# Kernel optimization log

Measured on AMD Instinct MI355X. Metric: run time of the kernel, lower is better.

Reference implementation:

```python
import jax, jax.numpy as jnp
import numpy as np

IMG_H, IMG_W = 240, 320
NEAR, FAR = 0.1, 10.0
CHUNK = 64  # triangles rasterized per scan step
CAM_K = np.array([[286.2057, 0.0, 162.6306],
                  [0.0, 286.7852, 121.0245],
                  [0.0, 0.0, 1.0]], np.float32)


def build_projection(cam, w, h, x0=0, y0=0, nc=NEAR, fc=FAR):
    q = -(fc + nc) / float(fc - nc)
    qn = -2.0 * fc * nc / float(fc - nc)
    proj = np.array([
        [2 * cam[0, 0] / w, -2 * cam[0, 1] / w, (-2 * cam[0, 2] + w + 2 * x0) / w, 0],
        [0, -2 * cam[1, 1] / h, (-2 * cam[1, 2] + h + 2 * y0) / h, 0],
        [0, 0, q, qn],
        [0, 0, -1, 0]], dtype=np.float64)
    proj[1, :] *= -1.0
    return jnp.asarray(proj.T, jnp.float32)


def vertex_normals(verts, faces):
    # per-face normal scattered to its vertices then renormalized
    # (equals dirt lighting.vertex_normals_pre_split on split meshes)
    v0, v1, v2 = verts[faces[:, 0]], verts[faces[:, 1]], verts[faces[:, 2]]
    fn = jnp.cross(v1 - v0, v2 - v0)
    fn = fn / jnp.maximum(jnp.linalg.norm(fn, axis=1, keepdims=True), 1e-12)
    vn = (jnp.zeros_like(verts)
          .at[faces[:, 0]].add(fn)
          .at[faces[:, 1]].add(fn)
          .at[faces[:, 2]].add(fn))
    return vn / jnp.maximum(jnp.linalg.norm(vn, axis=1, keepdims=True), 1e-12)


def transform_vertices(vertices, pose, faces, proj):
    vert_obj = jnp.concatenate([vertices, jnp.ones_like(vertices[:, -1:])], axis=1)  # [V,4]
    normals = vertex_normals(vert_obj[:, :3], faces)
    gl = jnp.array([[1., 0., 0.], [0., -1., 0.], [0., 0., -1.]], jnp.float32)
    rot = gl @ pose[:3, :3]
    # replicate the flat-list surgery: cam_pose[:3,:3]=gl@R, negate t_y, t_z
    cam_pose = pose.at[:3, :3].set(rot).at[1, 3].multiply(-1.0).at[2, 3].multiply(-1.0)
    view = cam_pose.T
    vert_cam = vert_obj @ view                                   # [V,4]
    vert_3d = vert_obj[:, :3] @ pose[:3, :3].T + pose[:3, 3]     # [V,3]
    vert_clip = vert_cam @ proj                                  # [V,4]
    return vert_obj, vert_3d, vert_clip, normals


def rasterise(vert_clip, colors, faces, H, W):
    # z-buffered triangle rasterization with perspective-correct barycentric
    # interpolation, processed in chunks of CHUNK triangles via lax.scan.
    eps = 1e-9
    wc = vert_clip[:, 3]
    inv_w = 1.0 / jnp.where(jnp.abs(wc) > eps, wc, eps)
    ndc = vert_clip[:, :3] * inv_w[:, None]
    px = (ndc[:, 0] + 1.0) * 0.5 * W   # screen x
    py = (1.0 - ndc[:, 1]) * 0.5 * H   # screen y (row 0 at top)
    pz = ndc[:, 2]

    tpx, tpy, tpz = px[faces], py[faces], pz[faces]   # [F,3]
    tiw = inv_w[faces]                                # [F,3]
    tcol = colors[faces]                              # [F,3,C]
    tval = jnp.all(wc[faces] > 1e-6, axis=1)          # all verts in front

    F = faces.shape[0]
    pad = (-F) % CHUNK
    def padf(a):
        if pad == 0:
            return a
        return jnp.concatenate([a, jnp.zeros((pad,) + a.shape[1:], a.dtype)], 0)
    tpx, tpy, tpz, tiw, tcol = padf(tpx), padf(tpy), padf(tpz), padf(tiw), padf(tcol)
    tval = padf(tval)
    n_steps = (F + pad) // CHUNK
    resh = lambda a: a.reshape((n_steps, CHUNK) + a.shape[1:])
    xs = tuple(map(resh, (tpx, tpy, tpz, tiw, tcol, tval)))

    Xg = (jnp.arange(W, dtype=jnp.float32) + 0.5)[None, :, None]  # pixel centers
    Yg = (jnp.arange(H, dtype=jnp.float32) + 0.5)[:, None, None]
    BIG = jnp.float32(1e9)

    def step(carry, chunk):
        zbuf, cbuf = carry
        cpx, cpy, cpz, ciw, ccol, cval = chunk
        ax, ay = cpx[:, 0], cpy[:, 0]
        bx, by = cpx[:, 1], cpy[:, 1]
        cx, cy = cpx[:, 2], cpy[:, 2]
        area = (bx - ax) * (cy - ay) - (by - ay) * (cx - ax)            # [Fc]
        inv_area = 1.0 / jnp.where(jnp.abs(area) > 1e-12, area, 1e-12)
        # normalized edge functions (barycentrics), [H,W,Fc]
        e0 = ((Xg - bx) * (cy - by) - (Yg - by) * (cx - bx)) * inv_area
        e1 = ((Xg - cx) * (ay - cy) - (Yg - cy) * (ax - cx)) * inv_area
        e2 = 1.0 - e0 - e1
        depth = e0 * cpz[:, 0] + e1 * cpz[:, 1] + e2 * cpz[:, 2]        # screen-linear z
        inside = ((e0 >= 0) & (e1 >= 0) & (e2 >= 0) & cval
                  & (jnp.abs(area) > 1e-12) & (depth >= -1.0) & (depth <= 1.0))
        dmask = jnp.where(inside, depth, BIG)
        best = jnp.argmin(dmask, axis=2)                                # [H,W]
        bidx = best[..., None]
        bdepth = jnp.take_along_axis(dmask, bidx, 2)[..., 0]
        take = bdepth < zbuf
        b0 = jnp.take_along_axis(e0, bidx, 2)[..., 0]
        b1 = jnp.take_along_axis(e1, bidx, 2)[..., 0]
        b2 = 1.0 - b0 - b1
        piw = jnp.stack([b0, b1, b2], -1) * ciw[best]                   # [H,W,3]
        den = jnp.sum(piw, -1, keepdims=True)
        den = jnp.where(jnp.abs(den) > 1e-12, den, 1e-12)
        col = jnp.einsum('hwk,hwkc->hwc', piw / den, ccol[best])        # persp-correct
        zbuf = jnp.where(take, bdepth, zbuf)
        cbuf = jnp.where(take[..., None], col, cbuf)
        return (zbuf, cbuf), None

    zbuf0 = jnp.full((H, W), BIG, jnp.float32)
    cbuf0 = jnp.zeros((H, W, colors.shape[1]), jnp.float32)
    (_, cbuf), _ = jax.lax.scan(jax.checkpoint(step), (zbuf0, cbuf0), xs)
    return cbuf


def setup_inputs() -> dict:
    key = jax.random.key(0)
    k1, k2 = jax.random.split(key)
    V, F = 12288, 4096
    vertices = 0.15 * jax.random.normal(k1, (1, V, 3), jnp.float32)
    faces = jax.random.randint(k2, (1, F, 3), 0, V, jnp.int32)
    pose = jnp.eye(4, dtype=jnp.float32).at[2, 3].set(0.6)  # object 0.6m in front
    return {"vertices": vertices, "faces": faces, "poses": pose[None]}


def reference(vertices, faces, poses):
    proj = build_projection(CAM_K, IMG_W, IMG_H)
    faces0 = jnp.asarray(faces[0], jnp.int32)
    vert_obj, vert_3d, vert_clip, normals = transform_vertices(vertices[0], poses[0], faces0, proj)
    colors = jnp.concatenate(
        [jnp.ones_like(vert_obj[:, :1]), vert_3d, normals, vert_obj], axis=1)  # [V,11]
    g = rasterise(vert_clip, colors, faces0, IMG_H, IMG_W)  # [H,W,11]
    return g[None]
```

## Files before the change

kernel.cpp:

```cpp
#include <hip/hip_runtime.h>
#include <math.h>

#pragma clang fp contract(off)

#define IMG_H 240
#define IMG_W 320
#define NPX   (IMG_H * IMG_W)
#define NCH   11
#define NCHP  12
#define NSLICE 16
#define CULL_M 1e-3f
#define EZ_M   1e-5f

struct ProjM { float m[16]; };

extern "C" __global__ void k_init(float* __restrict__ vnacc, int n3v,
                                  unsigned long long* __restrict__ zkey) {
  int i = blockIdx.x * 256 + threadIdx.x;
  if (i < n3v) vnacc[i] = 0.0f;
  if (i < NPX) zkey[i] = ~0ull;
}

__device__ __forceinline__ void xform(float x, float y, float z,
                                      const float* __restrict__ pose,
                                      const ProjM& P,
                                      float& px, float& py, float& pz,
                                      float& iw, float& wc) {
  float c0 = ((x*pose[0]     + y*pose[1])     + z*pose[2])     + pose[3];
  float c1 = ((x*(-pose[4])  + y*(-pose[5]))  + z*(-pose[6]))  + (-pose[7]);
  float c2 = ((x*(-pose[8])  + y*(-pose[9]))  + z*(-pose[10])) + (-pose[11]);
  float c3 = ((x*pose[12]    + y*pose[13])    + z*pose[14])    + pose[15];
  float q0 = ((c0*P.m[0]  + c1*P.m[1])  + c2*P.m[2])  + c3*P.m[3];
  float q1 = ((c0*P.m[4]  + c1*P.m[5])  + c2*P.m[6])  + c3*P.m[7];
  float q2 = ((c0*P.m[8]  + c1*P.m[9])  + c2*P.m[10]) + c3*P.m[11];
  float q3 = ((c0*P.m[12] + c1*P.m[13]) + c2*P.m[14]) + c3*P.m[15];
  wc = q3;
  float denw = (fabsf(wc) > 1e-9f) ? wc : 1e-9f;
  iw = 1.0f / denw;
  float ndx = q0 * iw, ndy = q1 * iw;
  pz = q2 * iw;
  px = ((ndx + 1.0f) * 0.5f) * (float)IMG_W;
  py = ((1.0f - ndy) * 0.5f) * (float)IMG_H;
}

extern "C" __global__ void k_face(const float* __restrict__ verts,
                                  const int* __restrict__ faces,
                                  const float* __restrict__ pose,
                                  ProjM P,
                                  float* __restrict__ vnacc,
                                  float4* __restrict__ frec,
                                  float4* __restrict__ fbb,
                                  float4* __restrict__ fe,
                                  int4*  __restrict__ fidx, int F) {
  int f = blockIdx.x * 64 + threadIdx.x;
  if (f >= F) return;
  int i0 = faces[3*f+0], i1 = faces[3*f+1], i2 = faces[3*f+2];
  float x0 = verts[3*i0+0], y0 = verts[3*i0+1], z0 = verts[3*i0+2];
  float x1 = verts[3*i1+0], y1 = verts[3*i1+1], z1 = verts[3*i1+2];
  float x2 = verts[3*i2+0], y2 = verts[3*i2+1], z2 = verts[3*i2+2];

  {
    float ux = x1 - x0, uy = y1 - y0, uz = z1 - z0;
    float vx = x2 - x0, vy = y2 - y0, vz = z2 - z0;
    float fx = uy*vz - uz*vy;
    float fy = uz*vx - ux*vz;
    float fz = ux*vy - uy*vx;
    float n = sqrtf((fx*fx + fy*fy) + fz*fz);
    float d = fmaxf(n, 1e-12f);
    fx = fx / d; fy = fy / d; fz = fz / d;
    atomicAdd(&vnacc[3*i0+0], fx); atomicAdd(&vnacc[3*i0+1], fy); atomicAdd(&vnacc[3*i0+2], fz);
    atomicAdd(&vnacc[3*i1+0], fx); atomicAdd(&vnacc[3*i1+1], fy); atomicAdd(&vnacc[3*i1+2], fz);
    atomicAdd(&vnacc[3*i2+0], fx); atomicAdd(&vnacc[3*i2+1], fy); atomicAdd(&vnacc[3*i2+2], fz);
  }

  float ax, ay, pz0, iw0, w0;  xform(x0, y0, z0, pose, P, ax, ay, pz0, iw0, w0);
  float bx, by, pz1, iw1, w1;  xform(x1, y1, z1, pose, P, bx, by, pz1, iw1, w1);
  float cx, cy, pz2, iw2, w2;  xform(x2, y2, z2, pose, P, cx, cy, pz2, iw2, w2);

  float area = (bx - ax) * (cy - ay) - (by - ay) * (cx - ax);
  float inva = 1.0f / ((fabsf(area) > 1e-12f) ? area : 1e-12f);
  bool valid = (w0 > 1e-6f) && (w1 > 1e-6f) && (w2 > 1e-6f) && (fabsf(area) > 1e-12f);
  float rax = 2.0f*cx - ax, ray = 2.0f*cy - ay;
  float rbx = 2.0f*cx - bx, rby = 2.0f*cy - by;
  float minx = fminf(cx, fminf(rax, rbx)), maxx = fmaxf(cx, fmaxf(rax, rbx));
  float miny = fminf(cy, fminf(ray, rby)), maxy = fmaxf(cy, fmaxf(ray, rby));
  frec[4*f+0] = make_float4(bx, by, cy - by, cx - bx);
  frec[4*f+1] = make_float4(cx, cy, ay - cy, ax - cx);
  frec[4*f+2] = make_float4(inva, pz0, pz1, pz2);
  frec[4*f+3] = make_float4(iw0, iw1, iw2, 0.0f);
  fbb[f] = valid ? make_float4(minx, maxx, miny, maxy)
                 : make_float4(1e30f, -1e30f, 1e30f, -1e30f);
  fidx[f] = make_int4(i0, i1, i2, 0);
  {
    double dbx = bx, dby = by, dcx = cx, dcy = cy, dax = ax, day = ay;
    double dinv = (double)inva;
    double d0 = dcy - dby, d1 = dcx - dbx;
    double d2 = day - dcy, d3 = dax - dcx;
    double a0 = d0 * dinv, b0 = -d1 * dinv, c0 = (dby * d1 - dbx * d0) * dinv;
    double a1 = d2 * dinv, b1 = -d3 * dinv, c1 = (dcy * d3 - dcx * d2) * dinv;
    fe[2*f+0] = make_float4((float)a0, (float)b0, (float)c0, 0.0f);
    fe[2*f+1] = make_float4((float)a1, (float)b1, (float)c1, 0.0f);
  }
}

extern "C" __global__ void k_vertex(const float* __restrict__ verts,
                                    const float* __restrict__ vnacc,
                                    const float* __restrict__ pose,
                                    float4* __restrict__ colors, int V) {
  int i = blockIdx.x * 64 + threadIdx.x;
  if (i >= V) return;
  float x = verts[3*i+0], y = verts[3*i+1], z = verts[3*i+2];

  float nx = vnacc[3*i+0], ny = vnacc[3*i+1], nz = vnacc[3*i+2];
  float nn = sqrtf((nx*nx + ny*ny) + nz*nz);
  float nm = fmaxf(nn, 1e-12f);
  nx = nx / nm; ny = ny / nm; nz = nz / nm;

  float v3x = ((x*pose[0] + y*pose[1]) + z*pose[2])  + pose[3];
  float v3y = ((x*pose[4] + y*pose[5]) + z*pose[6])  + pose[7];
  float v3z = ((x*pose[8] + y*pose[9]) + z*pose[10]) + pose[11];

  colors[3*i+0] = make_float4(1.0f, v3x, v3y, v3z);
  colors[3*i+1] = make_float4(nx, ny, nz, x);
  colors[3*i+2] = make_float4(y, z, 1.0f, 0.0f);
}

extern "C" __global__ __launch_bounds__(256)
void k_rasterA(const float4* __restrict__ frec,
               const float4* __restrict__ fbb,
               const float4* __restrict__ fe,
               unsigned long long* __restrict__ zkey,
               int F, int nslice) {
  int t = threadIdx.x;
  int wave = t >> 6;
  int lane = t & 63;
  int sx = (wave & 1) * 8, sy = (wave >> 1) * 8;
  int pxi = blockIdx.x * 16 + sx + (lane & 7);
  int pyi = blockIdx.y * 16 + sy + (lane >> 3);
  float X = (float)pxi + 0.5f;
  float Y = (float)pyi + 0.5f;
  float tXlo = (float)(blockIdx.x * 16 + sx) + 0.5f, tXhi = tXlo + 7.0f;
  float tYlo = (float)(blockIdx.y * 16 + sy) + 0.5f, tYhi = tYlo + 7.0f;

  int f0 = blockIdx.z * nslice;
  int f1 = min(F, f0 + nslice);

  float bestd = 1e9f;
  int   besti = -1;

  for (int base = f0; base < f1; base += 64) {
    int f = base + lane;
    bool ov = false;
    if (f < f1) {
      float4 bb = fbb[f];
      ov = (bb.x - 1.0f <= tXhi) && (bb.y + 1.0f >= tXlo) &&
           (bb.z - 1.0f <= tYhi) && (bb.w + 1.0f >= tYlo);
      if (ov) {
        float4 E0 = fe[2*f+0];
        float4 E1 = fe[2*f+1];
        float pa0 = E0.x * tXlo, pb0 = E0.x * tXhi;
        float qa0 = E0.y * tYlo, qb0 = E0.y * tYhi;
        float e0mx = (fmaxf(pa0, pb0) + fmaxf(qa0, qb0)) + E0.z;
        float e0mn = (fminf(pa0, pb0) + fminf(qa0, qb0)) + E0.z;
        float pa1 = E1.x * tXlo, pb1 = E1.x * tXhi;
        float qa1 = E1.y * tYlo, qb1 = E1.y * tYhi;
        float e1mx = (fmaxf(pa1, pb1) + fmaxf(qa1, qb1)) + E1.z;
        float e1mn = (fminf(pa1, pb1) + fminf(qa1, qb1)) + E1.z;
        float e2mx = (1.0f - e0mn) - e1mn;
        ov = (e0mx >= -CULL_M) && (e1mx >= -CULL_M) && (e2mx >= -CULL_M);
      }
    }
    unsigned long long mask = __ballot(ov);

    while (mask) {
      int j0 = __builtin_ctzll(mask);
      mask &= mask - 1;
      bool two = (mask != 0ull);
      int j1 = two ? __builtin_ctzll(mask) : j0;
      if (two) mask &= mask - 1;

      int ju0 = __builtin_amdgcn_readfirstlane(base + j0);
      int ju1 = __builtin_amdgcn_readfirstlane(base + j1);
      const float4* fr0 = frec + (size_t)ju0 * 4;
      const float4* fr1 = frec + (size_t)ju1 * 4;
      float4 C0 = fr0[2];
      float4 C1 = fr1[2];
      float zmin0 = fminf(C0.y, fminf(C0.z, C0.w));
      float zmin1 = fminf(C1.y, fminf(C1.z, C1.w));
      float zmg = two ? fminf(zmin0, zmin1) : zmin0;
      if (__ballot(bestd > zmg - EZ_M) == 0ull) continue;
      float4 A0 = fr0[0], B0 = fr0[1];
      float4 A1 = fr1[0], B1 = fr1[1];

      {
        float t0 = (X - A0.x) * A0.z;
        float t1 = (Y - A0.y) * A0.w;
        float e0 = (t0 - t1) * C0.x;
        float t2 = (X - B0.x) * B0.z;
        float t3 = (Y - B0.y) * B0.w;
        float e1 = (t2 - t3) * C0.x;
        float e2 = (1.0f - e0) - e1;
        float depth = ((e0 * C0.y) + (e1 * C0.z)) + (e2 * C0.w);
        bool inside = (e0 >= 0.0f) && (e1 >= 0.0f) && (e2 >= 0.0f) &&
                      (depth >= -1.0f) && (depth <= 1.0f);
        if (inside && depth < bestd) { bestd = depth; besti = ju0; }
      }
      if (two) {
        float t0 = (X - A1.x) * A1.z;
        float t1 = (Y - A1.y) * A1.w;
        float e0 = (t0 - t1) * C1.x;
        float t2 = (X - B1.x) * B1.z;
        float t3 = (Y - B1.y) * B1.w;
        float e1 = (t2 - t3) * C1.x;
        float e2 = (1.0f - e0) - e1;
        float depth = ((e0 * C1.y) + (e1 * C1.z)) + (e2 * C1.w);
        bool inside = (e0 >= 0.0f) && (e1 >= 0.0f) && (e2 >= 0.0f) &&
                      (depth >= -1.0f) && (depth <= 1.0f);
        if (inside && depth < bestd) { bestd = depth; besti = ju1; }
      }
    }
  }

  if (besti >= 0) {
    unsigned int ub = __float_as_uint(bestd);
    ub = (ub & 0x80000000u) ? ~ub : (ub | 0x80000000u);
    unsigned long long key = ((unsigned long long)ub << 32) | (unsigned int)besti;
    atomicMin(&zkey[(size_t)pyi * IMG_W + pxi], key);
  }
}

extern "C" __global__ __launch_bounds__(256)
void k_resolve(const unsigned long long* __restrict__ zkey,
               const float4* __restrict__ frec,
               const float4* __restrict__ colors,
               const int4* __restrict__ fidx,
               float* __restrict__ out) {
  __shared__ float sOut[256 * NCH];
  int t = threadIdx.x;
  int p = blockIdx.x * 256 + t;
  int pyi = p / IMG_W, pxi = p - pyi * IMG_W;
  float X = (float)pxi + 0.5f;
  float Y = (float)pyi + 0.5f;
  unsigned long long key = zkey[p];

  float oc[NCH];
  if (key != ~0ull) {
    int besti = (int)(key & 0xFFFFFFFFu);
    const float4* fr = frec + (size_t)besti * 4;
    float4 A = fr[0], B = fr[1], C = fr[2], D = fr[3];
    float t0 = (X - A.x) * A.z;
    float t1 = (Y - A.y) * A.w;
    float e0 = (t0 - t1) * C.x;
    float t2 = (X - B.x) * B.z;
    float t3 = (Y - B.y) * B.w;
    float e1 = (t2 - t3) * C.x;
    float b2 = (1.0f - e0) - e1;
    float p0 = e0 * D.x, p1 = e1 * D.y, p2 = b2 * D.z;
    float den = (p0 + p1) + p2;
    if (!(fabsf(den) > 1e-12f)) den = 1e-12f;
    float u0 = p0 / den, u1 = p1 / den, u2 = p2 / den;
    int4 vi = fidx[besti];
    float c0v[NCHP], c1v[NCHP], c2v[NCHP];
    #pragma unroll
    for (int k = 0; k < 3; ++k) {
      *(float4*)(c0v + 4*k) = colors[3*vi.x + k];
      *(float4*)(c1v + 4*k) = colors[3*vi.y + k];
      *(float4*)(c2v + 4*k) = colors[3*vi.z + k];
    }
    #pragma unroll
    for (int ch = 0; ch < NCH; ++ch)
      oc[ch] = (u0 * c0v[ch] + u1 * c1v[ch]) + u2 * c2v[ch];
  } else {
    #pragma unroll
    for (int ch = 0; ch < NCH; ++ch) oc[ch] = 0.0f;
  }
  #pragma unroll
  for (int ch = 0; ch < NCH; ++ch) sOut[t * NCH + ch] = oc[ch];
  __syncthreads();
  float4* o4 = (float4*)(out + (size_t)blockIdx.x * 256 * NCH);
  const float4* s4 = (const float4*)sOut;
  #pragma unroll
  for (int k = 0; k < 3; ++k) {
    int idx = t + k * 256;
    if (idx < 704) o4[idx] = s4[idx];
  }
}

extern "C" void kernel_launch(void* const* d_in, const int* in_sizes, int n_in,
                              void* d_out, int out_size, void* d_ws, size_t ws_size,
                              hipStream_t stream) {
  const float* verts = (const float*)d_in[0];
  const int*   faces = (const int*)d_in[1];
  const float* pose  = (const float*)d_in[2];
  float* out = (float*)d_out;
  int V = in_sizes[0] / 3;
  int F = in_sizes[1] / 3;

  float* ws = (float*)d_ws;
  size_t o = 0;
  auto alloc = [&](size_t n) { size_t r = o; o += (n + 3) & ~(size_t)3; return r; };
  size_t o_zk   = alloc((size_t)2 * NPX);
  size_t o_vn   = alloc((size_t)3 * V);
  size_t o_col  = alloc((size_t)NCHP * V);
  size_t o_fr   = alloc((size_t)16 * F);
  size_t o_bb   = alloc((size_t)4 * F);
  size_t o_fe   = alloc((size_t)8 * F);
  size_t o_fi   = alloc((size_t)4 * F);
  unsigned long long* zkey = (unsigned long long*)(ws + o_zk);
  float*  vnacc = ws + o_vn;
  float4* col   = (float4*)(ws + o_col);
  float4* frec  = (float4*)(ws + o_fr);
  float4* fbb   = (float4*)(ws + o_bb);
  float4* fe    = (float4*)(ws + o_fe);
  int4*   fidx  = (int4*)(ws + o_fi);

  double fxd = 286.2057, sd = 0.0, cxd = 162.6306;
  double fyd = 286.7852, cyd = 121.0245;
  double wd = IMG_W, hd = IMG_H, ncd = 0.1, fcd = 10.0;
  double q  = -(fcd + ncd) / (fcd - ncd);
  double qn = -2.0 * fcd * ncd / (fcd - ncd);
  double Pd[16] = {
    2.0*fxd/wd, -2.0*sd/wd, (-2.0*cxd + wd)/wd, 0.0,
    0.0,        2.0*fyd/hd, (2.0*cyd - hd)/hd, -0.0,
    0.0,        0.0,        q,                  qn,
    0.0,        0.0,       -1.0,                0.0 };
  ProjM P;
  for (int i = 0; i < 16; ++i) P.m[i] = (float)Pd[i];

  int n3v = 3 * V;
  int initN = (NPX > n3v) ? NPX : n3v;
  k_init<<<(initN + 255) / 256, 256, 0, stream>>>(vnacc, n3v, zkey);
  k_face<<<(F + 63) / 64, 64, 0, stream>>>(verts, faces, pose, P, vnacc,
                                           frec, fbb, fe, fidx, F);
  k_vertex<<<(V + 63) / 64, 64, 0, stream>>>(verts, vnacc, pose, col, V);
  int nslice = (F + NSLICE - 1) / NSLICE;
  dim3 g(IMG_W / 16, IMG_H / 16, NSLICE);
  k_rasterA<<<g, 256, 0, stream>>>(frec, fbb, fe, zkey, F, nslice);
  k_resolve<<<NPX / 256, 256, 0, stream>>>(zkey, frec, col, fidx, out);
}
```

Baseline: 90.64 us.

## Add block-level face binning in rasterizer and fuse vertex attributes into resolve

The rasterizer now culls faces once per 16x16 block using all 256 threads, compacts the survivors into a shared-memory list, and then has each 8x8 wave re-test only that short list. The face slice count drops from 16 to 4, so each block handles more faces and fewer blocks are launched. The separate vertex-color kernel is removed and the resolve kernel computes normalized normals and pose-transformed positions on the fly for the three vertices it needs. This saves one launch and the color buffer traffic, at the cost of extra __syncthreads per batch, repeated per-pixel vertex math, and less grid parallelism.

```diff
diff --git a/kernel.cpp b/kernel.cpp
--- a/kernel.cpp
+++ b/kernel.cpp
@@ -7,8 +7,7 @@
 #define IMG_W 320
 #define NPX   (IMG_H * IMG_W)
 #define NCH   11
-#define NCHP  12
-#define NSLICE 16
+#define NSLICE 4
 #define CULL_M 1e-3f
 #define EZ_M   1e-5f
 
@@ -103,34 +102,14 @@
   }
 }
 
-extern "C" __global__ void k_vertex(const float* __restrict__ verts,
-                                    const float* __restrict__ vnacc,
-                                    const float* __restrict__ pose,
-                                    float4* __restrict__ colors, int V) {
-  int i = blockIdx.x * 64 + threadIdx.x;
-  if (i >= V) return;
-  float x = verts[3*i+0], y = verts[3*i+1], z = verts[3*i+2];
-
-  float nx = vnacc[3*i+0], ny = vnacc[3*i+1], nz = vnacc[3*i+2];
-  float nn = sqrtf((nx*nx + ny*ny) + nz*nz);
-  float nm = fmaxf(nn, 1e-12f);
-  nx = nx / nm; ny = ny / nm; nz = nz / nm;
-
-  float v3x = ((x*pose[0] + y*pose[1]) + z*pose[2])  + pose[3];
-  float v3y = ((x*pose[4] + y*pose[5]) + z*pose[6])  + pose[7];
-  float v3z = ((x*pose[8] + y*pose[9]) + z*pose[10]) + pose[11];
-
-  colors[3*i+0] = make_float4(1.0f, v3x, v3y, v3z);
-  colors[3*i+1] = make_float4(nx, ny, nz, x);
-  colors[3*i+2] = make_float4(y, z, 1.0f, 0.0f);
-}
-
 extern "C" __global__ __launch_bounds__(256)
 void k_rasterA(const float4* __restrict__ frec,
                const float4* __restrict__ fbb,
                const float4* __restrict__ fe,
                unsigned long long* __restrict__ zkey,
                int F, int nslice) {
+  __shared__ int sList[256];
+  __shared__ int sWaveCnt[4];
   int t = threadIdx.x;
   int wave = t >> 6;
   int lane = t & 63;
@@ -141,6 +120,8 @@
   float Y = (float)pyi + 0.5f;
   float tXlo = (float)(blockIdx.x * 16 + sx) + 0.5f, tXhi = tXlo + 7.0f;
   float tYlo = (float)(blockIdx.y * 16 + sy) + 0.5f, tYhi = tYlo + 7.0f;
+  float bXlo = (float)(blockIdx.x * 16) + 0.5f, bXhi = bXlo + 15.0f;
+  float bYlo = (float)(blockIdx.y * 16) + 0.5f, bYhi = bYlo + 15.0f;
 
   int f0 = blockIdx.z * nslice;
   int f1 = min(F, f0 + nslice);
@@ -148,77 +129,115 @@
   float bestd = 1e9f;
   int   besti = -1;
 
-  for (int base = f0; base < f1; base += 64) {
-    int f = base + lane;
-    bool ov = false;
+  for (int base = f0; base < f1; base += 256) {
+    int f = base + t;
+    bool bp = false;
     if (f < f1) {
       float4 bb = fbb[f];
-      ov = (bb.x - 1.0f <= tXhi) && (bb.y + 1.0f >= tXlo) &&
-           (bb.z - 1.0f <= tYhi) && (bb.w + 1.0f >= tYlo);
-      if (ov) {
+      bp = (bb.x - 1.0f <= bXhi) && (bb.y + 1.0f >= bXlo) &&
+           (bb.z - 1.0f <= bYhi) && (bb.w + 1.0f >= bYlo);
+      if (bp) {
         float4 E0 = fe[2*f+0];
         float4 E1 = fe[2*f+1];
-        float pa0 = E0.x * tXlo, pb0 = E0.x * tXhi;
-        float qa0 = E0.y * tYlo, qb0 = E0.y * tYhi;
+        float pa0 = E0.x * bXlo, pb0 = E0.x * bXhi;
+        float qa0 = E0.y * bYlo, qb0 = E0.y * bYhi;
         float e0mx = (fmaxf(pa0, pb0) + fmaxf(qa0, qb0)) + E0.z;
         float e0mn = (fminf(pa0, pb0) + fminf(qa0, qb0)) + E0.z;
-        float pa1 = E1.x * tXlo, pb1 = E1.x * tXhi;
-        float qa1 = E1.y * tYlo, qb1 = E1.y * tYhi;
+        float pa1 = E1.x * bXlo, pb1 = E1.x * bXhi;
+        float qa1 = E1.y * bYlo, qb1 = E1.y * bYhi;
         float e1mx = (fmaxf(pa1, pb1) + fmaxf(qa1, qb1)) + E1.z;
         float e1mn = (fminf(pa1, pb1) + fminf(qa1, qb1)) + E1.z;
         float e2mx = (1.0f - e0mn) - e1mn;
-        ov = (e0mx >= -CULL_M) && (e1mx >= -CULL_M) && (e2mx >= -CULL_M);
+        bp = (e0mx >= -CULL_M) && (e1mx >= -CULL_M) && (e2mx >= -CULL_M);
       }
     }
-    unsigned long long mask = __ballot(ov);
-
-    while (mask) {
-      int j0 = __builtin_ctzll(mask);
-      mask &= mask - 1;
-      bool two = (mask != 0ull);
-      int j1 = two ? __builtin_ctzll(mask) : j0;
-      if (two) mask &= mask - 1;
-
-      int ju0 = __builtin_amdgcn_readfirstlane(base + j0);
-      int ju1 = __builtin_amdgcn_readfirstlane(base + j1);
-      const float4* fr0 = frec + (size_t)ju0 * 4;
-      const float4* fr1 = frec + (size_t)ju1 * 4;
-      float4 C0 = fr0[2];
-      float4 C1 = fr1[2];
-      float zmin0 = fminf(C0.y, fminf(C0.z, C0.w));
-      float zmin1 = fminf(C1.y, fminf(C1.z, C1.w));
-      float zmg = two ? fminf(zmin0, zmin1) : zmin0;
-      if (__ballot(bestd > zmg - EZ_M) == 0ull) continue;
-      float4 A0 = fr0[0], B0 = fr0[1];
-      float4 A1 = fr1[0], B1 = fr1[1];
-
-      {
-        float t0 = (X - A0.x) * A0.z;
-        float t1 = (Y - A0.y) * A0.w;
-        float e0 = (t0 - t1) * C0.x;
-        float t2 = (X - B0.x) * B0.z;
-        float t3 = (Y - B0.y) * B0.w;
-        float e1 = (t2 - t3) * C0.x;
-        float e2 = (1.0f - e0) - e1;
-        float depth = ((e0 * C0.y) + (e1 * C0.z)) + (e2 * C0.w);
-        bool inside = (e0 >= 0.0f) && (e1 >= 0.0f) && (e2 >= 0.0f) &&
-                      (depth >= -1.0f) && (depth <= 1.0f);
-        if (inside && depth < bestd) { bestd = depth; besti = ju0; }
+    unsigned long long wm = __ballot(bp);
+    if (lane == 0) sWaveCnt[wave] = __popcll(wm);
+    __syncthreads();
+    int c0 = sWaveCnt[0], c1 = sWaveCnt[1], c2 = sWaveCnt[2], c3 = sWaveCnt[3];
+    int tot = ((c0 + c1) + c2) + c3;
+    if (bp) {
+      int off = (wave > 0 ? c0 : 0) + (wave > 1 ? c1 : 0) + (wave > 2 ? c2 : 0);
+      int pos = off + __popcll(wm & ((1ull << lane) - 1ull));
+      sList[pos] = f;
+    }
+    __syncthreads();
+
+    for (int k0 = 0; k0 < tot; k0 += 64) {
+      int k = k0 + lane;
+      bool ov = false;
+      int fi = 0;
+      if (k < tot) {
+        fi = sList[k];
+        float4 bb = fbb[fi];
+        ov = (bb.x - 1.0f <= tXhi) && (bb.y + 1.0f >= tXlo) &&
+             (bb.z - 1.0f <= tYhi) && (bb.w + 1.0f >= tYlo);
+        if (ov) {
+          float4 E0 = fe[2*fi+0];
+          float4 E1 = fe[2*fi+1];
+          float pa0 = E0.x * tXlo, pb0 = E0.x * tXhi;
+          float qa0 = E0.y * tYlo, qb0 = E0.y * tYhi;
+          float e0mx = (fmaxf(pa0, pb0) + fmaxf(qa0, qb0)) + E0.z;
+          float e0mn = (fminf(pa0, pb0) + fminf(qa0, qb0)) + E0.z;
+          float pa1 = E1.x * tXlo, pb1 = E1.x * tXhi;
+          float qa1 = E1.y * tYlo, qb1 = E1.y * tYhi;
+          float e1mx = (fmaxf(pa1, pb1) + fmaxf(qa1, qb1)) + E1.z;
+          float e1mn = (fminf(pa1, pb1) + fminf(qa1, qb1)) + E1.z;
+          float e2mx = (1.0f - e0mn) - e1mn;
+          ov = (e0mx >= -CULL_M) && (e1mx >= -CULL_M) && (e2mx >= -CULL_M);
+        }
       }
-      if (two) {
-        float t0 = (X - A1.x) * A1.z;
-        float t1 = (Y - A1.y) * A1.w;
-        float e0 = (t0 - t1) * C1.x;
-        float t2 = (X - B1.x) * B1.z;
-        float t3 = (Y - B1.y) * B1.w;
-        float e1 = (t2 - t3) * C1.x;
-        float e2 = (1.0f - e0) - e1;
-        float depth = ((e0 * C1.y) + (e1 * C1.z)) + (e2 * C1.w);
-        bool inside = (e0 >= 0.0f) && (e1 >= 0.0f) && (e2 >= 0.0f) &&
-                      (depth >= -1.0f) && (depth <= 1.0f);
-        if (inside && depth < bestd) { bestd = depth; besti = ju1; }
+      unsigned long long mask = __ballot(ov);
+
+      while (mask) {
+        int j0 = __builtin_ctzll(mask);
+        mask &= mask - 1;
+        bool two = (mask != 0ull);
+        int j1 = two ? __builtin_ctzll(mask) : j0;
+        if (two) mask &= mask - 1;
+
+        int ju0 = __builtin_amdgcn_readfirstlane(__shfl(fi, j0));
+        int ju1 = __builtin_amdgcn_readfirstlane(__shfl(fi, j1));
+        const float4* fr0 = frec + (size_t)ju0 * 4;
+        const float4* fr1 = frec + (size_t)ju1 * 4;
+        float4 C0 = fr0[2];
+        float4 C1 = fr1[2];
+        float zmin0 = fminf(C0.y, fminf(C0.z, C0.w));
+        float zmin1 = fminf(C1.y, fminf(C1.z, C1.w));
+        float zmg = two ? fminf(zmin0, zmin1) : zmin0;
+        if (__ballot(bestd > zmg - EZ_M) == 0ull) continue;
+        float4 A0 = fr0[0], B0 = fr0[1];
+        float4 A1 = fr1[0], B1 = fr1[1];
+
+        {
+          float t0 = (X - A0.x) * A0.z;
+          float t1 = (Y - A0.y) * A0.w;
+          float e0 = (t0 - t1) * C0.x;
+          float t2 = (X - B0.x) * B0.z;
+          float t3 = (Y - B0.y) * B0.w;
+          float e1 = (t2 - t3) * C0.x;
+          float e2 = (1.0f - e0) - e1;
+          float depth = ((e0 * C0.y) + (e1 * C0.z)) + (e2 * C0.w);
+          bool inside = (e0 >= 0.0f) && (e1 >= 0.0f) && (e2 >= 0.0f) &&
+                        (depth >= -1.0f) && (depth <= 1.0f);
+          if (inside && depth < bestd) { bestd = depth; besti = ju0; }
+        }
+        if (two) {
+          float t0 = (X - A1.x) * A1.z;
+          float t1 = (Y - A1.y) * A1.w;
+          float e0 = (t0 - t1) * C1.x;
+          float t2 = (X - B1.x) * B1.z;
+          float t3 = (Y - B1.y) * B1.w;
+          float e1 = (t2 - t3) * C1.x;
+          float e2 = (1.0f - e0) - e1;
+          float depth = ((e0 * C1.y) + (e1 * C1.z)) + (e2 * C1.w);
+          bool inside = (e0 >= 0.0f) && (e1 >= 0.0f) && (e2 >= 0.0f) &&
+                        (depth >= -1.0f) && (depth <= 1.0f);
+          if (inside && depth < bestd) { bestd = depth; besti = ju1; }
+        }
       }
     }
+    __syncthreads();
   }
 
   if (besti >= 0) {
@@ -232,8 +251,10 @@
 extern "C" __global__ __launch_bounds__(256)
 void k_resolve(const unsigned long long* __restrict__ zkey,
                const float4* __restrict__ frec,
-               const float4* __restrict__ colors,
                const int4* __restrict__ fidx,
+               const float* __restrict__ verts,
+               const float* __restrict__ vnacc,
+               const float* __restrict__ pose,
                float* __restrict__ out) {
   __shared__ float sOut[256 * NCH];
   int t = threadIdx.x;
@@ -260,16 +281,27 @@
     if (!(fabsf(den) > 1e-12f)) den = 1e-12f;
     float u0 = p0 / den, u1 = p1 / den, u2 = p2 / den;
     int4 vi = fidx[besti];
-    float c0v[NCHP], c1v[NCHP], c2v[NCHP];
+
+    float cv[3][NCH];
+    int vids[3] = { vi.x, vi.y, vi.z };
     #pragma unroll
     for (int k = 0; k < 3; ++k) {
-      *(float4*)(c0v + 4*k) = colors[3*vi.x + k];
-      *(float4*)(c1v + 4*k) = colors[3*vi.y + k];
-      *(float4*)(c2v + 4*k) = colors[3*vi.z + k];
+      int id = vids[k];
+      float x = verts[3*id+0], y = verts[3*id+1], z = verts[3*id+2];
+      float nx = vnacc[3*id+0], ny = vnacc[3*id+1], nz = vnacc[3*id+2];
+      float nn = sqrtf((nx*nx + ny*ny) + nz*nz);
+      float nm = fmaxf(nn, 1e-12f);
+      nx = nx / nm; ny = ny / nm; nz = nz / nm;
+      float v3x = ((x*pose[0] + y*pose[1]) + z*pose[2])  + pose[3];
+      float v3y = ((x*pose[4] + y*pose[5]) + z*pose[6])  + pose[7];
+      float v3z = ((x*pose[8] + y*pose[9]) + z*pose[10]) + pose[11];
+      cv[k][0] = 1.0f;  cv[k][1] = v3x; cv[k][2] = v3y; cv[k][3] = v3z;
+      cv[k][4] = nx;    cv[k][5] = ny;  cv[k][6] = nz;
+      cv[k][7] = x;     cv[k][8] = y;   cv[k][9] = z;   cv[k][10] = 1.0f;
     }
     #pragma unroll
     for (int ch = 0; ch < NCH; ++ch)
-      oc[ch] = (u0 * c0v[ch] + u1 * c1v[ch]) + u2 * c2v[ch];
+      oc[ch] = (u0 * cv[0][ch] + u1 * cv[1][ch]) + u2 * cv[2][ch];
   } else {
     #pragma unroll
     for (int ch = 0; ch < NCH; ++ch) oc[ch] = 0.0f;
@@ -301,14 +333,12 @@
   auto alloc = [&](size_t n) { size_t r = o; o += (n + 3) & ~(size_t)3; return r; };
   size_t o_zk   = alloc((size_t)2 * NPX);
   size_t o_vn   = alloc((size_t)3 * V);
-  size_t o_col  = alloc((size_t)NCHP * V);
   size_t o_fr   = alloc((size_t)16 * F);
   size_t o_bb   = alloc((size_t)4 * F);
   size_t o_fe   = alloc((size_t)8 * F);
   size_t o_fi   = alloc((size_t)4 * F);
   unsigned long long* zkey = (unsigned long long*)(ws + o_zk);
   float*  vnacc = ws + o_vn;
-  float4* col   = (float4*)(ws + o_col);
   float4* frec  = (float4*)(ws + o_fr);
   float4* fbb   = (float4*)(ws + o_bb);
   float4* fe    = (float4*)(ws + o_fe);
@@ -332,9 +362,9 @@
   k_init<<<(initN + 255) / 256, 256, 0, stream>>>(vnacc, n3v, zkey);
   k_face<<<(F + 63) / 64, 64, 0, stream>>>(verts, faces, pose, P, vnacc,
                                            frec, fbb, fe, fidx, F);
-  k_vertex<<<(V + 63) / 64, 64, 0, stream>>>(verts, vnacc, pose, col, V);
   int nslice = (F + NSLICE - 1) / NSLICE;
   dim3 g(IMG_W / 16, IMG_H / 16, NSLICE);
   k_rasterA<<<g, 256, 0, stream>>>(frec, fbb, fe, zkey, F, nslice);
-  k_resolve<<<NPX / 256, 256, 0, stream>>>(zkey, frec, col, fidx, out);
-}
+  k_resolve<<<NPX / 256, 256, 0, stream>>>(zkey, frec, fidx, verts, vnacc,
+                                           pose, out);
+}
```

Result: faster. 87.81 us (-3.1%).
